# Performance work log

Hardware: AMD Instinct MI355X
Metric: run time of the kernel (lower is better)

Reference implementation:

```python
import jax, jax.numpy as jnp
import numpy as np

EPS = 1e-7
FEAT_DIM = 128
N_DATA = 100000
NCE_K = 16384
NCE_T = 0.07


def _l2norm(x):
    # Normalize(power=2): x / (sum(x^2, axis=1)^(1/2))
    return x / jnp.sqrt(jnp.sum(x * x, axis=1, keepdims=True))


def _embed(x, W, b):
    return _l2norm(x @ W.T + b)


def _contrast_loss(x, n_data):
    # x: [B, K+1] of (unnormalized) probabilities; col 0 = positive
    bsz = x.shape[0]
    m = x.shape[1] - 1
    Pn = 1.0 / float(n_data)
    c = m * Pn + EPS
    log_D1 = jnp.log(x[:, 0] / (x[:, 0] + c))          # positives
    log_D0 = jnp.log((m * Pn) / (x[:, 1:] + c))         # negatives
    return -(log_D1.sum() + log_D0.sum()) / bsz


def setup_inputs() -> dict:
    key = jax.random.key(0)
    ks = jax.random.split(key, 10)
    s_dim, t_dim = 1024, 2048
    B = 64
    stdv = 1.0 / np.sqrt(FEAT_DIM / 3.0)
    inp = {
        "f_s": jax.random.normal(ks[0], (B, s_dim), dtype=jnp.float32),
        "f_t": jax.random.normal(ks[1], (B, t_dim), dtype=jnp.float32),
        "idx": jax.random.randint(ks[2], (B,), 0, N_DATA),
        "contrast_idx": jax.random.randint(ks[3], (B, NCE_K + 1), 0, N_DATA),
        # Embed params (linear): Linear(dim_in, feat_dim)
        "Ws": jax.random.normal(ks[4], (FEAT_DIM, s_dim), dtype=jnp.float32) / np.sqrt(s_dim),
        "bs": jnp.zeros((FEAT_DIM,), dtype=jnp.float32),
        "Wt": jax.random.normal(ks[5], (FEAT_DIM, t_dim), dtype=jnp.float32) / np.sqrt(t_dim),
        "bt": jnp.zeros((FEAT_DIM,), dtype=jnp.float32),
        # memory banks, init uniform(-stdv, stdv) as in CRD ContrastMemory
        "memory_v1": jax.random.uniform(ks[6], (N_DATA, FEAT_DIM), jnp.float32, -stdv, stdv),
        "memory_v2": jax.random.uniform(ks[7], (N_DATA, FEAT_DIM), jnp.float32, -stdv, stdv),
    }
    return inp


def reference(f_s, f_t, idx, contrast_idx, Ws, bs, Wt, bt, memory_v1, memory_v2):
    v_s = _embed(f_s, Ws, bs)   # [B, D]
    v_t = _embed(f_t, Wt, bt)   # [B, D]

    # idx.select(1,0).copy_(y): column 0 is the positive index
    idx_all = jnp.concatenate([idx[:, None], contrast_idx[:, 1:]], axis=1)  # [B, K+1]

    # gather from memory banks + bmm similarity
    w1 = memory_v1[idx_all]   # [B, K+1, D] (v_t side bank)
    w2 = memory_v2[idx_all]   # [B, K+1, D] (v_s side bank)
    out_t = jnp.exp(jnp.einsum('bkd,bd->bk', w1, v_t) / NCE_T)  # out_v2
    out_s = jnp.exp(jnp.einsum('bkd,bd->bk', w2, v_s) / NCE_T)  # out_v1

    # Z set on first batch: Z = out.mean() * n_data (detached constant)
    Z_s = jax.lax.stop_gradient(out_s.mean()) * N_DATA
    Z_t = jax.lax.stop_gradient(out_t.mean()) * N_DATA
    out_s = out_s / Z_s
    out_t = out_t / Z_t

    s_loss = _contrast_loss(out_s, N_DATA)
    t_loss = _contrast_loss(out_t, N_DATA)
    return s_loss + t_loss
```

## Files before the change

kernel.cpp:

```cpp
#include <hip/hip_runtime.h>

#define NDATA 100000
#define KP1 16385
#define BSZ 64
#define PTOT (BSZ * KP1)
#define NTILES 1563
#define INV_T (1.0f / 0.07f)

typedef short short8 __attribute__((ext_vector_type(8)));
typedef float f32x4 __attribute__((ext_vector_type(4)));

__device__ __forceinline__ float wave_reduce64(float v) {
    #pragma unroll
    for (int off = 32; off >= 1; off >>= 1) v += __shfl_xor(v, off);
    return v;
}

__device__ __forceinline__ unsigned short f2bf(float f) {
    unsigned u = __float_as_uint(f);
    u += 0x7FFFu + ((u >> 16) & 1u);
    return (unsigned short)(u >> 16);
}

__device__ __forceinline__ float dot4(float4 a, float4 b, float acc) {
    acc = fmaf(a.x, b.x, acc);
    acc = fmaf(a.y, b.y, acc);
    acc = fmaf(a.z, b.z, acc);
    return fmaf(a.w, b.w, acc);
}

__global__ __launch_bounds__(256) void embed_kernel(
    const float* __restrict__ fs, const float* __restrict__ ft,
    const float* __restrict__ Ws, const float* __restrict__ bs,
    const float* __restrict__ Wt, const float* __restrict__ bt,
    float* __restrict__ vraw_s, float* __restrict__ vraw_t,
    float* __restrict__ n2s, float* __restrict__ n2t)
{
    __shared__ __align__(16) float4 FS[512];
    __shared__ __align__(16) float4 FT[1024];

    const int t  = threadIdx.x;
    const int dt = blockIdx.x;
    const int b0 = blockIdx.y * 2;

    for (int q = t; q < 512; q += 256) {
        const int b = q >> 8, i = q & 255;
        FS[q] = ((const float4*)(fs + (size_t)(b0 + b) * 1024))[i];
    }
    for (int q = t; q < 1024; q += 256) {
        const int b = q >> 9, i = q & 511;
        FT[q] = ((const float4*)(ft + (size_t)(b0 + b) * 2048))[i];
    }
    __syncthreads();

    const int w = t >> 6, lane = t & 63;
    float ps0 = 0.0f, ps1 = 0.0f, pt0 = 0.0f, pt1 = 0.0f;

    #pragma unroll
    for (int r = 0; r < 4; ++r) {
        const int d = dt * 16 + w * 4 + r;
        const float4* wrow = (const float4*)(Ws + (size_t)d * 1024);
        float a0 = 0.0f, a1 = 0.0f;
        #pragma unroll
        for (int i = 0; i < 4; ++i) {
            const float4 wv = wrow[i * 64 + lane];
            a0 = dot4(wv, FS[i * 64 + lane], a0);
            a1 = dot4(wv, FS[256 + i * 64 + lane], a1);
        }
        a0 = wave_reduce64(a0) + bs[d];
        a1 = wave_reduce64(a1) + bs[d];
        ps0 = fmaf(a0, a0, ps0);
        ps1 = fmaf(a1, a1, ps1);
        if (lane == 0) {
            vraw_s[(size_t)b0 * 128 + d]       = a0;
            vraw_s[(size_t)(b0 + 1) * 128 + d] = a1;
        }
    }
    #pragma unroll
    for (int r = 0; r < 4; ++r) {
        const int d = dt * 16 + w * 4 + r;
        const float4* wrow = (const float4*)(Wt + (size_t)d * 2048);
        float a0 = 0.0f, a1 = 0.0f;
        #pragma unroll
        for (int i = 0; i < 8; ++i) {
            const float4 wv = wrow[i * 64 + lane];
            a0 = dot4(wv, FT[i * 64 + lane], a0);
            a1 = dot4(wv, FT[512 + i * 64 + lane], a1);
        }
        a0 = wave_reduce64(a0) + bt[d];
        a1 = wave_reduce64(a1) + bt[d];
        pt0 = fmaf(a0, a0, pt0);
        pt1 = fmaf(a1, a1, pt1);
        if (lane == 0) {
            vraw_t[(size_t)b0 * 128 + d]       = a0;
            vraw_t[(size_t)(b0 + 1) * 128 + d] = a1;
        }
    }
    if (lane == 0) {
        atomicAdd(&n2s[b0],     ps0);
        atomicAdd(&n2s[b0 + 1], ps1);
        atomicAdd(&n2t[b0],     pt0);
        atomicAdd(&n2t[b0 + 1], pt1);
    }
}

__device__ __forceinline__ void stage_tile(
    unsigned short* __restrict__ dst, const float* __restrict__ src,
    int row0, int t, bool clampRows)
{
    #pragma unroll
    for (int i = 0; i < 8; ++i) {
        const int q = t + i * 256;
        const int r = q >> 5, c = q & 31;
        int gr = row0 + r;
        if (clampRows && gr >= NDATA) gr = NDATA - 1;
        const float4 v = ((const float4*)(src + (size_t)gr * 128))[c];
        ushort4 u;
        u.x = f2bf(v.x); u.y = f2bf(v.y); u.z = f2bf(v.z); u.w = f2bf(v.w);
        *(ushort4*)&dst[r * 128 + (((c >> 1) ^ (r & 15)) * 8) + (c & 1) * 4] = u;
    }
}

__global__ __launch_bounds__(256) void sgemm_kernel(
    const float* __restrict__ m1, const float* __restrict__ m2,
    const float* __restrict__ vraw_s, const float* __restrict__ vraw_t,
    float* __restrict__ S1, float* __restrict__ S2)
{
    __shared__ __align__(16) unsigned short Vs[64 * 128];
    __shared__ __align__(16) unsigned short As[2][64 * 128];

    const int t = threadIdx.x;
    const int bank = blockIdx.y;
    const float* __restrict__ bankp = bank ? m2 : m1;
    const float* __restrict__ vp    = bank ? vraw_s : vraw_t;
    float* __restrict__ Sp          = bank ? S2 : S1;

    const int tile0  = blockIdx.x * 4;
    const int ntiles = min(4, NTILES - tile0);

    stage_tile(Vs, vp, 0, t, false);
    stage_tile(As[0], bankp, tile0 * 64, t, true);
    __syncthreads();

    const int lane = t & 63;
    const int m  = lane & 15;
    const int q4 = lane >> 4;
    const int m0 = (t >> 6) * 16;

    for (int it = 0; it < ntiles; ++it) {
        if (it + 1 < ntiles)
            stage_tile(As[(it + 1) & 1], bankp, (tile0 + it + 1) * 64, t, true);

        const unsigned short* A = As[it & 1];
        const int row0 = (tile0 + it) * 64;

        short8 af[4];
        #pragma unroll
        for (int kk = 0; kk < 4; ++kk)
            af[kk] = *(const short8*)&A[(m0 + m) * 128 + (((kk * 4 + q4) ^ m) * 8)];

        const int rbase = row0 + m0 + q4 * 4;
        const bool valid = (rbase < NDATA);

        #pragma unroll
        for (int n0 = 0; n0 < 64; n0 += 16) {
            f32x4 acc = {0.f, 0.f, 0.f, 0.f};
            #pragma unroll
            for (int kk = 0; kk < 4; ++kk) {
                short8 bf = *(const short8*)&Vs[(n0 + m) * 128 + (((kk * 4 + q4) ^ m) * 8)];
                acc = __builtin_amdgcn_mfma_f32_16x16x32_bf16(af[kk], bf, acc, 0, 0, 0);
            }
            if (valid)
                *(f32x4*)(Sp + (size_t)(n0 + m) * NDATA + rbase) = acc;
        }
        __syncthreads();
    }
}

__global__ __launch_bounds__(256) void gather_kernel(
    const int* __restrict__ cidx,
    const float* __restrict__ S1, const float* __restrict__ S2,
    const float* __restrict__ n2t, const float* __restrict__ n2s,
    float* __restrict__ acc)
{
    const int b = blockIdx.x, part = blockIdx.y, t = threadIdx.x;
    const float sct = INV_T * rsqrtf(n2t[b]);
    const float scs = INV_T * rsqrtf(n2s[b]);
    const float* __restrict__ S1b = S1 + (size_t)b * NDATA;
    const float* __restrict__ S2b = S2 + (size_t)b * NDATA;
    const int kbase = part * 2048 + 1;

    int rows[8];
    #pragma unroll
    for (int j = 0; j < 8; ++j)
        rows[j] = cidx[(size_t)b * KP1 + kbase + j * 256 + t];

    float v1[8], v2[8];
    #pragma unroll
    for (int j = 0; j < 8; ++j) {
        v1[j] = S1b[rows[j]];
        v2[j] = S2b[rows[j]];
    }

    float seT = 0.f, se2T = 0.f, seS = 0.f, se2S = 0.f;
    #pragma unroll
    for (int j = 0; j < 8; ++j) {
        const float e1 = __expf(v1[j] * sct);
        const float e2 = __expf(v2[j] * scs);
        seT += e1; se2T = fmaf(e1, e1, se2T);
        seS += e2; se2S = fmaf(e2, e2, se2S);
    }

    seT = wave_reduce64(seT);  se2T = wave_reduce64(se2T);
    seS = wave_reduce64(seS);  se2S = wave_reduce64(se2S);

    __shared__ float red[4][4];
    if ((t & 63) == 0) {
        const int w = t >> 6;
        red[w][0] = seT; red[w][1] = se2T; red[w][2] = seS; red[w][3] = se2S;
    }
    __syncthreads();
    if (t < 4)
        atomicAdd(&acc[t], red[0][t] + red[1][t] + red[2][t] + red[3][t]);
}

__global__ __launch_bounds__(64) void final_kernel(
    const int* __restrict__ idx,
    const float* __restrict__ S1, const float* __restrict__ S2,
    const float* __restrict__ n2t, const float* __restrict__ n2s,
    const float* __restrict__ acc, float* __restrict__ out)
{
    const int b = threadIdx.x;
    const float c = 0.16384f + 1e-7f;
    const int row = idx[b];

    const float e1p = __expf(S1[(size_t)b * NDATA + row] * INV_T * rsqrtf(n2t[b]));
    const float e2p = __expf(S2[(size_t)b * NDATA + row] * INV_T * rsqrtf(n2s[b]));

    const float pseT = wave_reduce64(e1p);
    const float pseS = wave_reduce64(e2p);

    const float seT_neg = acc[0], se2T_neg = acc[1];
    const float seS_neg = acc[2], se2S_neg = acc[3];

    const float zn = (float)PTOT / (float)NDATA;
    const float invZt = zn / (seT_neg + pseT);
    const float invZs = zn / (seS_neg + pseS);

    const float PB = (float)(PTOT - BSZ);
    const float LOG_MPN_C = -6.1035156e-7f;
    const float ic = 1.0f / c;

    const float negT = PB * LOG_MPN_C
                     - seT_neg * invZt * ic
                     + 0.5f * se2T_neg * invZt * invZt * ic * ic;
    const float negS = PB * LOG_MPN_C
                     - seS_neg * invZs * ic
                     + 0.5f * se2S_neg * invZs * invZs * ic * ic;

    const float x0t = e1p * invZt, x0s = e2p * invZs;
    float pos = __logf(x0t / (x0t + c)) + __logf(x0s / (x0s + c));
    pos = wave_reduce64(pos);

    if (b == 0) out[0] = -(negT + negS + pos) * (1.0f / 64.0f);
}

extern "C" void kernel_launch(void* const* d_in, const int* in_sizes, int n_in,
                              void* d_out, int out_size, void* d_ws, size_t ws_size,
                              hipStream_t stream) {
    const float* fs   = (const float*)d_in[0];
    const float* ft   = (const float*)d_in[1];
    const int*   idx  = (const int*)d_in[2];
    const int*   cidx = (const int*)d_in[3];
    const float* Ws   = (const float*)d_in[4];
    const float* bs   = (const float*)d_in[5];
    const float* Wt   = (const float*)d_in[6];
    const float* bt   = (const float*)d_in[7];
    const float* m1   = (const float*)d_in[8];
    const float* m2   = (const float*)d_in[9];
    float* out = (float*)d_out;

    float* ws     = (float*)d_ws;
    float* n2t    = ws;
    float* n2s    = ws + 64;
    float* acc    = ws + 128;
    float* vraw_s = ws + 144;
    float* vraw_t = vraw_s + 8192;
    float* S1     = vraw_t + 8192;
    float* S2     = S1 + (size_t)BSZ * NDATA;

    hipMemsetAsync(ws, 0, 144 * sizeof(float), stream);

    embed_kernel<<<dim3(8, 32), dim3(256), 0, stream>>>(
        fs, ft, Ws, bs, Wt, bt, vraw_s, vraw_t, n2s, n2t);
    sgemm_kernel<<<dim3(391, 2), dim3(256), 0, stream>>>(
        m1, m2, vraw_s, vraw_t, S1, S2);
    gather_kernel<<<dim3(64, 8), dim3(256), 0, stream>>>(
        cidx, S1, S2, n2t, n2s, acc);
    final_kernel<<<dim3(1), dim3(64), 0, stream>>>(
        idx, S1, S2, n2t, n2s, acc, out);
}
```

Before: 203.2 us.

## Drop LDS staging in bank GEMM; load MFMA fragments directly from global

The sgemm kernel no longer stages 64-row tiles of the memory bank and the query vectors through shared memory with barriers. Each wave now keeps the bf16 B fragments for all 64 queries in registers and walks 16-row chunks of the bank with a grid-stride loop, loading A fragments straight from global and converting them in registers. This removes LDS traffic and __syncthreads from the bandwidth-bound bank scan, at the cost of more registers and less explicit prefetch overlap. The gather kernel is also split into twice as many blocks, each doing half the work, to raise parallelism.

```diff
diff --git a/kernel.cpp b/kernel.cpp
--- a/kernel.cpp
+++ b/kernel.cpp
@@ -4,7 +4,7 @@
 #define KP1 16385
 #define BSZ 64
 #define PTOT (BSZ * KP1)
-#define NTILES 1563
+#define NCHUNKS 6250
 #define INV_T (1.0f / 0.07f)
 
 typedef short short8 __attribute__((ext_vector_type(8)));
@@ -20,6 +20,15 @@
     unsigned u = __float_as_uint(f);
     u += 0x7FFFu + ((u >> 16) & 1u);
     return (unsigned short)(u >> 16);
+}
+
+__device__ __forceinline__ short8 pack_bf16(float4 lo, float4 hi) {
+    short8 r;
+    r[0] = (short)f2bf(lo.x); r[1] = (short)f2bf(lo.y);
+    r[2] = (short)f2bf(lo.z); r[3] = (short)f2bf(lo.w);
+    r[4] = (short)f2bf(hi.x); r[5] = (short)f2bf(hi.y);
+    r[6] = (short)f2bf(hi.z); r[7] = (short)f2bf(hi.w);
+    return r;
 }
 
 __device__ __forceinline__ float dot4(float4 a, float4 b, float acc) {
@@ -104,76 +113,60 @@
     }
 }
 
-__device__ __forceinline__ void stage_tile(
-    unsigned short* __restrict__ dst, const float* __restrict__ src,
-    int row0, int t, bool clampRows)
-{
-    #pragma unroll
-    for (int i = 0; i < 8; ++i) {
-        const int q = t + i * 256;
-        const int r = q >> 5, c = q & 31;
-        int gr = row0 + r;
-        if (clampRows && gr >= NDATA) gr = NDATA - 1;
-        const float4 v = ((const float4*)(src + (size_t)gr * 128))[c];
-        ushort4 u;
-        u.x = f2bf(v.x); u.y = f2bf(v.y); u.z = f2bf(v.z); u.w = f2bf(v.w);
-        *(ushort4*)&dst[r * 128 + (((c >> 1) ^ (r & 15)) * 8) + (c & 1) * 4] = u;
-    }
-}
-
 __global__ __launch_bounds__(256) void sgemm_kernel(
     const float* __restrict__ m1, const float* __restrict__ m2,
     const float* __restrict__ vraw_s, const float* __restrict__ vraw_t,
     float* __restrict__ S1, float* __restrict__ S2)
 {
-    __shared__ __align__(16) unsigned short Vs[64 * 128];
-    __shared__ __align__(16) unsigned short As[2][64 * 128];
-
     const int t = threadIdx.x;
     const int bank = blockIdx.y;
     const float* __restrict__ bankp = bank ? m2 : m1;
     const float* __restrict__ vp    = bank ? vraw_s : vraw_t;
     float* __restrict__ Sp          = bank ? S2 : S1;
 
-    const int tile0  = blockIdx.x * 4;
-    const int ntiles = min(4, NTILES - tile0);
-
-    stage_tile(Vs, vp, 0, t, false);
-    stage_tile(As[0], bankp, tile0 * 64, t, true);
-    __syncthreads();
-
     const int lane = t & 63;
     const int m  = lane & 15;
     const int q4 = lane >> 4;
-    const int m0 = (t >> 6) * 16;
-
-    for (int it = 0; it < ntiles; ++it) {
-        if (it + 1 < ntiles)
-            stage_tile(As[(it + 1) & 1], bankp, (tile0 + it + 1) * 64, t, true);
-
-        const unsigned short* A = As[it & 1];
-        const int row0 = (tile0 + it) * 64;
-
+
+    short8 bf[4][4];
+    #pragma unroll
+    for (int n = 0; n < 4; ++n) {
+        const float4* vrow = (const float4*)(vp + (size_t)(n * 16 + m) * 128);
+        #pragma unroll
+        for (int kk = 0; kk < 4; ++kk) {
+            const float4 lo = vrow[(kk * 4 + q4) * 2];
+            const float4 hi = vrow[(kk * 4 + q4) * 2 + 1];
+            bf[n][kk] = pack_bf16(lo, hi);
+        }
+    }
+
+    const int wave   = (blockIdx.x << 2) | (t >> 6);
+    const int nwaves = gridDim.x << 2;
+
+    for (int cid = wave; cid < NCHUNKS; cid += nwaves) {
+        const int row0 = cid << 4;
+        const float4* arow = (const float4*)(bankp + (size_t)(row0 + m) * 128);
+
+        float4 a[8];
+        #pragma unroll
+        for (int kk = 0; kk < 4; ++kk) {
+            a[kk * 2]     = arow[(kk * 4 + q4) * 2];
+            a[kk * 2 + 1] = arow[(kk * 4 + q4) * 2 + 1];
+        }
         short8 af[4];
         #pragma unroll
         for (int kk = 0; kk < 4; ++kk)
-            af[kk] = *(const short8*)&A[(m0 + m) * 128 + (((kk * 4 + q4) ^ m) * 8)];
-
-        const int rbase = row0 + m0 + q4 * 4;
-        const bool valid = (rbase < NDATA);
-
-        #pragma unroll
-        for (int n0 = 0; n0 < 64; n0 += 16) {
+            af[kk] = pack_bf16(a[kk * 2], a[kk * 2 + 1]);
+
+        const size_t cbase = (size_t)row0 + q4 * 4;
+        #pragma unroll
+        for (int n = 0; n < 4; ++n) {
             f32x4 acc = {0.f, 0.f, 0.f, 0.f};
             #pragma unroll
-            for (int kk = 0; kk < 4; ++kk) {
-                short8 bf = *(const short8*)&Vs[(n0 + m) * 128 + (((kk * 4 + q4) ^ m) * 8)];
-                acc = __builtin_amdgcn_mfma_f32_16x16x32_bf16(af[kk], bf, acc, 0, 0, 0);
-            }
-            if (valid)
-                *(f32x4*)(Sp + (size_t)(n0 + m) * NDATA + rbase) = acc;
-        }
-        __syncthreads();
+            for (int kk = 0; kk < 4; ++kk)
+                acc = __builtin_amdgcn_mfma_f32_16x16x32_bf16(af[kk], bf[n][kk], acc, 0, 0, 0);
+            *(f32x4*)(Sp + (size_t)(n * 16 + m) * NDATA + cbase) = acc;
+        }
     }
 }
 
@@ -188,23 +181,23 @@
     const float scs = INV_T * rsqrtf(n2s[b]);
     const float* __restrict__ S1b = S1 + (size_t)b * NDATA;
     const float* __restrict__ S2b = S2 + (size_t)b * NDATA;
-    const int kbase = part * 2048 + 1;
-
-    int rows[8];
-    #pragma unroll
-    for (int j = 0; j < 8; ++j)
+    const int kbase = part * 1024 + 1;
+
+    int rows[4];
+    #pragma unroll
+    for (int j = 0; j < 4; ++j)
         rows[j] = cidx[(size_t)b * KP1 + kbase + j * 256 + t];
 
-    float v1[8], v2[8];
-    #pragma unroll
-    for (int j = 0; j < 8; ++j) {
+    float v1[4], v2[4];
+    #pragma unroll
+    for (int j = 0; j < 4; ++j) {
         v1[j] = S1b[rows[j]];
         v2[j] = S2b[rows[j]];
     }
 
     float seT = 0.f, se2T = 0.f, seS = 0.f, se2S = 0.f;
     #pragma unroll
-    for (int j = 0; j < 8; ++j) {
+    for (int j = 0; j < 4; ++j) {
         const float e1 = __expf(v1[j] * sct);
         const float e2 = __expf(v2[j] * scs);
         seT += e1; se2T = fmaf(e1, e1, se2T);
@@ -293,9 +286,9 @@
 
     embed_kernel<<<dim3(8, 32), dim3(256), 0, stream>>>(
         fs, ft, Ws, bs, Wt, bt, vraw_s, vraw_t, n2s, n2t);
-    sgemm_kernel<<<dim3(391, 2), dim3(256), 0, stream>>>(
+    sgemm_kernel<<<dim3(384, 2), dim3(256), 0, stream>>>(
         m1, m2, vraw_s, vraw_t, S1, S2);
-    gather_kernel<<<dim3(64, 8), dim3(256), 0, stream>>>(
+    gather_kernel<<<dim3(64, 16), dim3(256), 0, stream>>>(
         cidx, S1, S2, n2t, n2s, acc);
     final_kernel<<<dim3(1), dim3(64), 0, stream>>>(
         idx, S1, S2, n2t, n2s, acc, out);
```

Result: slower. 207.4 us (+2.1%).
